# Kernel optimization log

Measured on AMD Instinct MI355X. Metric: run time of the kernel, lower is better.

The kernel has to match this reference:

```python
import jax, jax.numpy as jnp
import numpy as np

HID, H, D = 128, 4, 32
NB, NP, NC = 60000, 2000, 4000
EM, EP, EI = 150000, 300000, 150000


def segment_softmax(logits, seg, n):
    # logits: [E, H], seg: [E] destination ids
    m = jax.ops.segment_max(logits, seg, num_segments=n)
    m = jnp.where(jnp.isfinite(m), m, 0.0)  # guard empty segments
    e = jnp.exp(logits - m[seg])
    s = jax.ops.segment_sum(e, seg, num_segments=n)
    return e / (s[seg] + 1e-16)


def layer_norm(x, g, b):
    mu = x.mean(-1, keepdims=True)
    v = ((x - mu) ** 2).mean(-1, keepdims=True)
    return (x - mu) / jnp.sqrt(v + 1e-5) * g + b


def setup_inputs():
    key = jax.random.key(0)
    ks = jax.random.split(key, 40)
    i = iter(range(40))
    nrm = lambda shape, s=1.0: jax.random.normal(ks[next(i)], shape, jnp.float32) * s
    w = lambda shape: nrm(shape, 0.05)
    inp = {
        'x_ball': nrm((NB, HID)),
        'x_player': nrm((NP, HID)),
        'x_context': nrm((NC, HID)),
        'em': jnp.stack([jax.random.randint(ks[next(i)], (EM,), 0, NP),
                         jax.random.randint(ks[next(i)], (EM,), 0, NB)]),
        'ep': jnp.stack([jax.random.randint(ks[next(i)], (EP,), 0, NB),
                         jax.random.randint(ks[next(i)], (EP,), 0, NB)]),
        'ei': jnp.stack([jax.random.randint(ks[next(i)], (EI,), 0, NB),
                         jax.random.randint(ks[next(i)], (EI,), 0, NC)]),
        'ea_p': nrm((EP, 1)),
        # GATv2Conv (player -matchup-> ball)
        'g_Wl': w((HID, HID)), 'g_Wr': w((HID, HID)), 'g_att': w((H, D)), 'g_b': jnp.zeros((HID,), jnp.float32),
        # TransformerConv (ball -recent_precedes-> ball), edge_dim=1
        't_Wq': w((HID, HID)), 't_bq': jnp.zeros((HID,), jnp.float32),
        't_Wk': w((HID, HID)), 't_bk': jnp.zeros((HID,), jnp.float32),
        't_Wv': w((HID, HID)), 't_bv': jnp.zeros((HID,), jnp.float32),
        't_We': w((1, HID)),
        't_Wskip': w((HID, HID)), 't_bskip': jnp.zeros((HID,), jnp.float32),
        # SAGEConv mean (ball -informs-> context)
        's_Wl': w((HID, HID)), 's_bl': jnp.zeros((HID,), jnp.float32), 's_Wr': w((HID, HID)),
        # per-type LayerNorms (only applied to types produced by the conv)
        'ln_ball_g': jnp.ones((HID,), jnp.float32), 'ln_ball_b': jnp.zeros((HID,), jnp.float32),
        'ln_ctx_g': jnp.ones((HID,), jnp.float32), 'ln_ctx_b': jnp.zeros((HID,), jnp.float32),
    }
    return inp


def reference(x_ball, x_player, x_context, em, ep, ei, ea_p,
              g_Wl, g_Wr, g_att, g_b,
              t_Wq, t_bq, t_Wk, t_bk, t_Wv, t_bv, t_We, t_Wskip, t_bskip,
              s_Wl, s_bl, s_Wr,
              ln_ball_g, ln_ball_b, ln_ctx_g, ln_ctx_b):
    # ---- GATv2Conv: player -> ball ----
    src, dst = em[0], em[1]
    xl = (x_player @ g_Wl).reshape(NP, H, D)   # src transform
    xr = (x_ball @ g_Wr).reshape(NB, H, D)     # dst transform
    e = xl[src] + xr[dst]                      # [EM, H, D]
    e = jnp.where(e > 0, e, 0.2 * e)           # leaky_relu(0.2)
    logit = jnp.einsum('ehd,hd->eh', e, g_att)
    alpha = segment_softmax(logit, dst, NB)
    gat = jax.ops.segment_sum(xl[src] * alpha[..., None], dst, num_segments=NB)
    gat = gat.reshape(NB, HID) + g_b

    # ---- TransformerConv: ball -> ball, edge_dim=1 ----
    src, dst = ep[0], ep[1]
    q = (x_ball @ t_Wq + t_bq).reshape(NB, H, D)
    k = (x_ball @ t_Wk + t_bk).reshape(NB, H, D)
    v = (x_ball @ t_Wv + t_bv).reshape(NB, H, D)
    ee = (ea_p @ t_We).reshape(EP, H, D)       # lin_edge (no bias)
    kj = k[src] + ee
    logit = jnp.einsum('ehd,ehd->eh', q[dst], kj) / jnp.sqrt(jnp.float32(D))
    alpha = segment_softmax(logit, dst, NB)
    tr = jax.ops.segment_sum((v[src] + ee) * alpha[..., None], dst, num_segments=NB)
    tr = tr.reshape(NB, HID) + x_ball @ t_Wskip + t_bskip  # root/skip connection

    # ---- SAGEConv mean: ball -> context ----
    src, dst = ei[0], ei[1]
    summ = jax.ops.segment_sum(x_ball[src], dst, num_segments=NC)
    cnt = jax.ops.segment_sum(jnp.ones((EI,), jnp.float32), dst, num_segments=NC)
    mean = summ / jnp.maximum(cnt, 1.0)[:, None]
    sage = mean @ s_Wl + s_bl + x_context @ s_Wr

    # ---- HeteroConv aggr='sum' + residual + per-type LayerNorm ----
    ball_out = layer_norm(gat + tr + x_ball, ln_ball_g, ln_ball_b)
    ctx_out = layer_norm(sage + x_context, ln_ctx_g, ln_ctx_b)
    # 'player' receives no messages -> passed through unchanged
    return (ball_out, ctx_out, x_player)
```

## Files before the change

### kernel.cpp

```cpp
#include <hip/hip_runtime.h>
#include <hip/hip_bf16.h>

#define NB 60000
#define NP 2000
#define NC 4000
#define EM_N 150000
#define EP_N 300000
#define EI_N 150000
#define POOL_N (EM_N + EP_N + EI_N)
#define SEG_TOT (NB + NB + NC)
#define SCAN_BLK 1024
#define NPART ((SEG_TOT + SCAN_BLK - 1) / SCAN_BLK)
#define BALL_TILES ((NB + 63) / 64)
#define PLYR_TILES ((NP + 63) / 64)
#define CTX_TILES ((NC + 63) / 64)
#define TPB 4
#define BW_CH ((BALL_TILES + TPB - 1) / TPB)
#define PW_CH ((PLYR_TILES + TPB - 1) / TPB)
#define CW_CH ((CTX_TILES + TPB - 1) / TPB)
#define GEMM_BLKS (6 * BW_CH + PW_CH + CW_CH)
#define FILL_BLKS ((POOL_N + 255) / 256)
#define CONVB ((NB * 16 + 255) / 256)
#define CONVC ((NC * 16 + 255) / 256)
#define CONVP ((NP * 16 + 255) / 256)
#define HIST_BLKS (FILL_BLKS + CONVB + CONVC + CONVP)
#define BBALL ((NB + 3) / 4)

#define QSCALE (0.17677669529663687f * 1.4426950408889634f)
#define LOG2E 1.4426950408889634f

typedef __hip_bfloat16 bf16;
typedef unsigned int u32;
typedef __attribute__((ext_vector_type(8))) short s8v;
typedef __attribute__((ext_vector_type(4))) float f4v;

__device__ __forceinline__ short f2bs(float f) {
    bf16 h = __float2bfloat16(f);
    return __builtin_bit_cast(short, h);
}
__device__ __forceinline__ float bsToF(short s) {
    return __builtin_bit_cast(float, ((unsigned)(unsigned short)s) << 16);
}
__device__ __forceinline__ float loF(u32 v) { return bsToF((short)(v & 0xffff)); }
__device__ __forceinline__ float hiF(u32 v) { return bsToF((short)(v >> 16)); }
__device__ __forceinline__ u32 packbf(float a, float b) {
    return (u32)(unsigned short)f2bs(a) | ((u32)(unsigned short)f2bs(b) << 16);
}
__device__ __forceinline__ void gl_lds16(const void* g, void* l) {
    __builtin_amdgcn_global_load_lds((const __attribute__((address_space(1))) void*)g,
                                     (__attribute__((address_space(3))) void*)l, 16, 0, 0);
}

__global__ void hist_wt_copy_kernel(const int* __restrict__ em, const int* __restrict__ ep,
                                    const int* __restrict__ ei, int* __restrict__ counts,
                                    int* __restrict__ ranks,
                                    const float* __restrict__ W0, const float* __restrict__ W1,
                                    const float* __restrict__ W2, const float* __restrict__ W3,
                                    const float* __restrict__ W4, const float* __restrict__ W5,
                                    const float* __restrict__ W6, const float* __restrict__ W7,
                                    ushort* __restrict__ Wt,
                                    const float* __restrict__ x_ball, const float* __restrict__ x_context,
                                    const float* __restrict__ x_player,
                                    u32* __restrict__ xbB, u32* __restrict__ xbC, u32* __restrict__ xbP,
                                    float* __restrict__ out) {
    if (blockIdx.x >= FILL_BLKS) {
        int b2 = blockIdx.x - FILL_BLKS;
        if (b2 < CONVB) {
            int idx = b2 * 256 + threadIdx.x;
            const float4* p = (const float4*)(x_ball + (size_t)idx * 8);
            float4 u = p[0], v = p[1];
            ((uint4*)xbB)[idx] = make_uint4(packbf(u.x, u.y), packbf(u.z, u.w),
                                            packbf(v.x, v.y), packbf(v.z, v.w));
        } else if (b2 < CONVB + CONVC) {
            int idx = (b2 - CONVB) * 256 + threadIdx.x;
            const float4* p = (const float4*)(x_context + (size_t)idx * 8);
            float4 u = p[0], v = p[1];
            ((uint4*)xbC)[idx] = make_uint4(packbf(u.x, u.y), packbf(u.z, u.w),
                                            packbf(v.x, v.y), packbf(v.z, v.w));
        } else {
            int idx = (b2 - CONVB - CONVC) * 256 + threadIdx.x;
            const float4* p = (const float4*)(x_player + (size_t)idx * 8);
            float4 u = p[0], v = p[1];
            ((uint4*)xbP)[idx] = make_uint4(packbf(u.x, u.y), packbf(u.z, u.w),
                                            packbf(v.x, v.y), packbf(v.z, v.w));
            float4* po = (float4*)(out + (size_t)(NB + NC) * 128 + (size_t)idx * 8);
            po[0] = u; po[1] = v;
        }
        return;
    }
    int t = blockIdx.x * 256 + threadIdx.x;
    if (t < 8 * 16384) {
        int w = t >> 14, r = t & 16383, k = r >> 7, n = r & 127;
        const float* W = (w == 0) ? W0 : (w == 1) ? W1 : (w == 2) ? W2 : (w == 3) ? W3
                       : (w == 4) ? W4 : (w == 5) ? W5 : (w == 6) ? W6 : W7;
        int sc = (n >> 5) * 32 + ((n & 1) << 4) + ((n & 31) >> 1);
        Wt[w * 16384 + (k >> 3) * 1024 + sc * 8 + (k & 7)] = (unsigned short)f2bs(W[k * 128 + n]);
    }
    if (t < EM_N) ranks[t] = atomicAdd(&counts[em[EM_N + t]], 1);
    else if (t < EM_N + EP_N) ranks[t] = atomicAdd(&counts[NB + ep[EP_N + (t - EM_N)]], 1);
    else if (t < POOL_N) ranks[t] = atomicAdd(&counts[2 * NB + ei[EI_N + (t - EM_N - EP_N)]], 1);
}

__global__ void scan_fused_kernel(const int* __restrict__ counts, int* __restrict__ offsets,
                                  int* __restrict__ gbase) {
    __shared__ int sd[256];
    __shared__ int sbase;
    int b = blockIdx.x, tid = threadIdx.x;
    int base = b * SCAN_BLK + tid * 4;
    int v[4]; int ts = 0;
#pragma unroll
    for (int j = 0; j < 4; j++) { int idx = base + j; v[j] = (idx < SEG_TOT) ? counts[idx] : 0; ts += v[j]; }
    sd[tid] = ts;
    for (int off = 1; off < 256; off <<= 1) {
        __syncthreads(); int t = (tid >= off) ? sd[tid - off] : 0;
        __syncthreads(); sd[tid] += t;
    }
    __syncthreads();
    if (tid == 255) sbase = atomicAdd(gbase, sd[255]);
    __syncthreads();
    int run = sd[tid] - ts + sbase;
#pragma unroll
    for (int j = 0; j < 4; j++) {
        int idx = base + j;
        if (idx < SEG_TOT) offsets[idx] = run;
        run += v[j];
    }
}

__global__ __launch_bounds__(256) void gemm6_fill_kernel(
    const u32* __restrict__ xbB, const u32* __restrict__ xbP, const u32* __restrict__ xbC,
    const float* __restrict__ Aball, const float* __restrict__ Actx,
    const ushort* __restrict__ Wt,
    const float* __restrict__ bq, const float* __restrict__ bk,
    const float* __restrict__ bv_, const float* __restrict__ bskip, const float* __restrict__ bl,
    u32* __restrict__ xrP, u32* __restrict__ qP, u32* __restrict__ kvP,
    u32* __restrict__ skipP, u32* __restrict__ xlP, u32* __restrict__ xwP,
    u32* __restrict__ ctxlinP,
    const int* __restrict__ em, const int* __restrict__ ep, const int* __restrict__ ei,
    const float* __restrict__ ea_p, const int* __restrict__ offsets,
    const int* __restrict__ ranks, int2* __restrict__ pool) {
    __shared__ ushort lds[16384];
    if (blockIdx.x >= GEMM_BLKS) {
        int t = (blockIdx.x - GEMM_BLKS) * 256 + threadIdx.x;
        int seg, s; float ea = 0.f;
        if (t < EM_N) { s = em[t]; seg = em[EM_N + t]; }
        else if (t < EM_N + EP_N) { int e = t - EM_N; s = ep[e]; seg = NB + ep[EP_N + e]; ea = ea_p[e]; }
        else if (t < POOL_N) { int e = t - EM_N - EP_N; s = ei[e]; seg = 2 * NB + ei[EI_N + e]; }
        else return;
        int pos = offsets[seg] + ranks[t];
        pool[pos] = make_int2(s, __float_as_int(ea));
        return;
    }
    const int tid = threadIdx.x;
    const int lane = tid & 63;
    const int wv = tid >> 6;
    const int quad = lane >> 4, l16 = lane & 15;

    int bid = blockIdx.x;
    int w, tile0, ntiles, M;
    const u32* A;
    if (bid < 6 * BW_CH) {
        int widx = bid / BW_CH;
        w = (widx < 5) ? widx : 6;
        int chunk = bid - widx * BW_CH;
        tile0 = chunk * TPB; ntiles = min(TPB, BALL_TILES - tile0); M = NB; A = xbB;
    } else if (bid < 6 * BW_CH + PW_CH) {
        w = 5; int chunk = bid - 6 * BW_CH;
        tile0 = chunk * TPB; ntiles = min(TPB, PLYR_TILES - tile0); M = NP; A = xbP;
    } else {
        w = 7; int chunk = bid - 6 * BW_CH - PW_CH;
        tile0 = chunk * TPB; ntiles = min(TPB, CTX_TILES - tile0); M = NC; A = xbC;
    }
    u32* op; const float* bp = nullptr; const float* resid = nullptr; float scale = 1.f;
    int ostride = 64, omul = 1, ooff = 0;
    switch (w) {
        case 0: op = xrP; break;
        case 1: op = qP; bp = bq; scale = QSCALE; break;
        case 2: op = kvP; bp = bk; ostride = 128; omul = 2; ooff = 0; break;
        case 3: op = kvP; bp = bv_; ostride = 128; omul = 2; ooff = 1; break;
        case 4: op = skipP; bp = bskip; resid = Aball; break;
        case 5: op = xlP; break;
        case 6: op = xwP; break;
        default: op = ctxlinP; bp = bl; resid = Actx; break;
    }

    {
        const ushort* src = Wt + w * 16384;
#pragma unroll
        for (int p = 0; p < 8; p++)
            gl_lds16(src + (size_t)(p * 256 + tid) * 8, lds + p * 2048 + wv * 512);
    }

    float2 bias2[4];
#pragma unroll
    for (int t = 0; t < 4; t++)
        bias2[t] = bp ? ((const float2*)bp)[t * 16 + l16] : make_float2(0.f, 0.f);

    s8v aCur[4], aNext[4];
    {
        int r0 = tile0 * 64 + wv * 16 + l16; if (r0 >= M) r0 = M - 1;
        const s8v* ap = (const s8v*)(A + (size_t)r0 * 64 + quad * 4);
#pragma unroll
        for (int kt = 0; kt < 4; kt++) aCur[kt] = ap[kt * 4];
    }
    __syncthreads();

    for (int ti = 0; ti < ntiles; ti++) {
        int tilebase = (tile0 + ti) * 64;
        if (ti + 1 < ntiles) {
            int rn = tilebase + 64 + wv * 16 + l16; if (rn >= M) rn = M - 1;
            const s8v* ap = (const s8v*)(A + (size_t)rn * 64 + quad * 4);
#pragma unroll
            for (int kt = 0; kt < 4; kt++) aNext[kt] = ap[kt * 4];
        }
        const int mbase = tilebase + wv * 16;
#pragma unroll
        for (int t = 0; t < 4; t++) {
            f4v alo = {0.f, 0.f, 0.f, 0.f}, ahi = {0.f, 0.f, 0.f, 0.f};
#pragma unroll
            for (int kt = 0; kt < 4; kt++) {
                s8v blo = *(const s8v*)(lds + (kt * 4 + quad) * 1024 + (t * 32 + l16) * 8);
                s8v bhi = *(const s8v*)(lds + (kt * 4 + quad) * 1024 + (t * 32 + 16 + l16) * 8);
                alo = __builtin_amdgcn_mfma_f32_16x16x32_bf16(aCur[kt], blo, alo, 0, 0, 0);
                ahi = __builtin_amdgcn_mfma_f32_16x16x32_bf16(aCur[kt], bhi, ahi, 0, 0, 0);
            }
#pragma unroll
            for (int r = 0; r < 4; r++) {
                int row = mbase + quad * 4 + r;
                if (row < M) {
                    float vlo = (alo[r] + bias2[t].x) * scale;
                    float vhi = (ahi[r] + bias2[t].y) * scale;
                    if (resid) {
                        float2 x2 = ((const float2*)resid)[(size_t)row * 64 + t * 16 + l16];
                        vlo += x2.x; vhi += x2.y;
                    }
                    op[(size_t)row * ostride + (size_t)(t * 16 + l16) * omul + ooff] = packbf(vlo, vhi);
                }
            }
        }
#pragma unroll
        for (int i = 0; i < 4; i++) aCur[i] = aNext[i];
    }
}

__device__ __forceinline__ void gat_batch(const u32 xv[4], const bool ok[4],
                                          float xr0, float xr1, float attx, float atty,
                                          float& n0, float& n1, float& deg) {
    float p[4], xa[4], xb[4];
#pragma unroll
    for (int i = 0; i < 4; i++) {
        xa[i] = loF(xv[i]); xb[i] = hiF(xv[i]);
        float u0 = xa[i] + xr0; u0 = u0 > 0.f ? u0 : 0.2f * u0;
        float u1 = xb[i] + xr1; u1 = u1 > 0.f ? u1 : 0.2f * u1;
        p[i] = u0 * attx + u1 * atty;
    }
#pragma unroll
    for (int m = 1; m <= 8; m <<= 1) {
#pragma unroll
        for (int i = 0; i < 4; i++) p[i] += __shfl_xor(p[i], m);
    }
#pragma unroll
    for (int i = 0; i < 4; i++) {
        p[i] = ok[i] ? exp2f(p[i]) : 0.f;
        n0 += p[i] * xa[i]; n1 += p[i] * xb[i]; deg += p[i];
    }
}

__device__ __forceinline__ void tr_batch(const uint2 kv[4], const float ea[4], const bool ok[4],
                                         float q0, float q1, float dw,
                                         float& sv0, float& sv1, float& spe, float& det) {
    float p[4];
#pragma unroll
    for (int i = 0; i < 4; i++) p[i] = q0 * loF(kv[i].x) + q1 * hiF(kv[i].x);
#pragma unroll
    for (int m = 1; m <= 8; m <<= 1) {
#pragma unroll
        for (int i = 0; i < 4; i++) p[i] += __shfl_xor(p[i], m);
    }
#pragma unroll
    for (int i = 0; i < 4; i++) {
        p[i] = ok[i] ? exp2f(p[i] + ea[i] * dw) : 0.f;
        sv0 += p[i] * loF(kv[i].y); sv1 += p[i] * hiF(kv[i].y);
        spe += p[i] * ea[i]; det += p[i];
    }
}

__global__ __launch_bounds__(256) void ball_sage_kernel(
    const u32* __restrict__ xlP, const u32* __restrict__ xrP, const u32* __restrict__ qP,
    const uint2* __restrict__ kvP, const u32* __restrict__ skipP, const u32* __restrict__ xwP,
    const u32* __restrict__ ctxlinP,
    const float* __restrict__ g_att, const float* __restrict__ g_b, const float* __restrict__ We,
    const int* __restrict__ offsets, const int* __restrict__ counts,
    const int2* __restrict__ pool,
    const float* __restrict__ ln_g, const float* __restrict__ ln_b,
    const float* __restrict__ cg, const float* __restrict__ cb,
    float* __restrict__ out) {
    __shared__ float part[4][128];
    const int wv = threadIdx.x >> 6, l = threadIdx.x & 63;

    if (blockIdx.x >= BBALL) {
        int c = blockIdx.x - BBALL;
        int beg = offsets[2 * NB + c], cnt = counts[2 * NB + c];
        float s0 = 0.f, s1 = 0.f;
        int j = wv;
        if (j < cnt) {
            int i0 = pool[beg + j].x;
            int idx1 = (j + 4 < cnt) ? beg + j + 4 : 0;
            int i1 = pool[idx1].x;
            u32 x0 = xwP[(size_t)i0 * 64 + l];
            u32 x1 = xwP[(size_t)i1 * 64 + l];
            for (; j < cnt; j += 4) {
                int idx2 = (j + 8 < cnt) ? beg + j + 8 : 0;
                int i2 = pool[idx2].x;
                s0 += loF(x0); s1 += hiF(x0);
                x0 = x1;
                x1 = xwP[(size_t)i2 * 64 + l];
            }
        }
        part[wv][l * 2] = s0; part[wv][l * 2 + 1] = s1;
        __syncthreads();
        if (wv == 0) {
            float m = fmaxf((float)cnt, 1.f);
            u32 cl = ctxlinP[(size_t)c * 64 + l];
            float v0 = (part[0][l * 2] + part[1][l * 2] + part[2][l * 2] + part[3][l * 2]) / m + loF(cl);
            float v1 = (part[0][l * 2 + 1] + part[1][l * 2 + 1] + part[2][l * 2 + 1] + part[3][l * 2 + 1]) / m + hiF(cl);
            float s = v0 + v1;
#pragma unroll
            for (int m2 = 1; m2 <= 32; m2 <<= 1) s += __shfl_xor(s, m2);
            float mu = s * (1.f / 128.f);
            float d0 = v0 - mu, d1 = v1 - mu;
            float qv = d0 * d0 + d1 * d1;
#pragma unroll
            for (int m2 = 1; m2 <= 32; m2 <<= 1) qv += __shfl_xor(qv, m2);
            float inv = rsqrtf(qv * (1.f / 128.f) + 1e-5f);
            float2 g2 = ((const float2*)cg)[l];
            float2 b2 = ((const float2*)cb)[l];
            ((float2*)out)[(size_t)(NB + c) * 64 + l] =
                make_float2(d0 * inv * g2.x + b2.x, d1 * inv * g2.y + b2.y);
        }
        return;
    }

    const int d = blockIdx.x * 4 + wv;
    const size_t rowD = (size_t)d * 64;
    const int ds = __builtin_amdgcn_readfirstlane(d);

    u32 xr2 = xrP[rowD + l];
    u32 q2 = qP[rowD + l];
    u32 sk = skipP[rowD + l];

    const int begG = offsets[ds], cntG = counts[ds];
    const int begT = offsets[NB + ds], cntT = counts[NB + ds];
    int gS[8];
#pragma unroll
    for (int i = 0; i < 8; i++) { int idx = (i < cntG) ? begG + i : 0; gS[i] = pool[idx].x; }
    int tS[8]; float tE[8];
#pragma unroll
    for (int i = 0; i < 8; i++) {
        int idx = (i < cntT) ? begT + i : 0;
        int2 pr = pool[idx]; tS[i] = pr.x; tE[i] = __int_as_float(pr.y);
    }

    u32 gx[8];
    if (cntG > 0) {
#pragma unroll
        for (int i = 0; i < 4; i++) gx[i] = xlP[(size_t)gS[i] * 64 + l];
        if (cntG > 4) {
#pragma unroll
            for (int i = 4; i < 8; i++) gx[i] = xlP[(size_t)gS[i] * 64 + l];
        }
    }
    uint2 kva[8];
    if (cntT > 0) {
#pragma unroll
        for (int i = 0; i < 4; i++) kva[i] = kvP[(size_t)tS[i] * 64 + l];
        if (cntT > 4) {
#pragma unroll
            for (int i = 4; i < 8; i++) kva[i] = kvP[(size_t)tS[i] * 64 + l];
        }
    }

    float q0 = loF(q2), q1 = hiF(q2);
    float2 we = ((const float2*)We)[l];
    float dw = q0 * we.x + q1 * we.y;
#pragma unroll
    for (int m = 1; m <= 8; m <<= 1) dw += __shfl_xor(dw, m);

    float2 attv = ((const float2*)g_att)[l];
    float attx = attv.x * LOG2E, atty = attv.y * LOG2E;
    float xr0 = loF(xr2), xr1 = hiF(xr2);
    float n0 = 0.f, n1 = 0.f, deg = 0.f;
    if (cntG > 0) {
        bool ok[4];
#pragma unroll
        for (int i = 0; i < 4; i++) ok[i] = (i < cntG);
        gat_batch(&gx[0], ok, xr0, xr1, attx, atty, n0, n1, deg);
        if (cntG > 4) {
            bool ok2[4];
#pragma unroll
            for (int i = 0; i < 4; i++) ok2[i] = (4 + i < cntG);
            gat_batch(&gx[4], ok2, xr0, xr1, attx, atty, n0, n1, deg);
        }
        for (int j = 8; j < cntG; j += 4) {
            bool ok3[4]; u32 xv[4];
#pragma unroll
            for (int i = 0; i < 4; i++) {
                ok3[i] = (j + i < cntG);
                int idx = ok3[i] ? begG + j + i : 0;
                xv[i] = xlP[(size_t)pool[idx].x * 64 + l];
            }
            gat_batch(xv, ok3, xr0, xr1, attx, atty, n0, n1, deg);
        }
    }
    float gat0 = n0 / (deg + 1e-16f), gat1 = n1 / (deg + 1e-16f);

    float sv0 = 0.f, sv1 = 0.f, spe = 0.f, det = 0.f;
    if (cntT > 0) {
        bool ok[4];
#pragma unroll
        for (int i = 0; i < 4; i++) ok[i] = (i < cntT);
        tr_batch(&kva[0], &tE[0], ok, q0, q1, dw, sv0, sv1, spe, det);
        if (cntT > 4) {
            bool ok2[4];
#pragma unroll
            for (int i = 0; i < 4; i++) ok2[i] = (4 + i < cntT);
            tr_batch(&kva[4], &tE[4], ok2, q0, q1, dw, sv0, sv1, spe, det);
        }
        for (int j = 8; j < cntT; j += 4) {
            bool ok3[4]; uint2 kv[4]; float ea[4];
#pragma unroll
            for (int i = 0; i < 4; i++) {
                ok3[i] = (j + i < cntT);
                int idx = ok3[i] ? begT + j + i : 0;
                int2 pr = pool[idx];
                ea[i] = __int_as_float(pr.y);
                kv[i] = kvP[(size_t)pr.x * 64 + l];
            }
            tr_batch(kv, ea, ok3, q0, q1, dw, sv0, sv1, spe, det);
        }
    }
    float tr0 = (sv0 + spe * we.x) / (det + 1e-16f);
    float tr1 = (sv1 + spe * we.y) / (det + 1e-16f);

    float2 gb2 = ((const float2*)g_b)[l];
    float val0 = loF(sk) + gb2.x + gat0 + tr0;
    float val1 = hiF(sk) + gb2.y + gat1 + tr1;
    float s = val0 + val1;
#pragma unroll
    for (int m = 1; m <= 32; m <<= 1) s += __shfl_xor(s, m);
    float mu = s * (1.f / 128.f);
    float d0 = val0 - mu, d1 = val1 - mu;
    float qv = d0 * d0 + d1 * d1;
#pragma unroll
    for (int m = 1; m <= 32; m <<= 1) qv += __shfl_xor(qv, m);
    float inv = rsqrtf(qv * (1.f / 128.f) + 1e-5f);
    float2 g2 = ((const float2*)ln_g)[l];
    float2 b2 = ((const float2*)ln_b)[l];
    ((float2*)out)[rowD + l] = make_float2(d0 * inv * g2.x + b2.x, d1 * inv * g2.y + b2.y);
}

extern "C" void kernel_launch(void* const* d_in, const int* in_sizes, int n_in,
                              void* d_out, int out_size, void* d_ws, size_t ws_size,
                              hipStream_t stream) {
    const float* x_ball = (const float*)d_in[0];
    const float* x_player = (const float*)d_in[1];
    const float* x_context = (const float*)d_in[2];
    const int* em = (const int*)d_in[3];
    const int* ep = (const int*)d_in[4];
    const int* ei = (const int*)d_in[5];
    const float* ea_p = (const float*)d_in[6];
    const float* g_Wl = (const float*)d_in[7];
    const float* g_Wr = (const float*)d_in[8];
    const float* g_att = (const float*)d_in[9];
    const float* g_b = (const float*)d_in[10];
    const float* t_Wq = (const float*)d_in[11];
    const float* t_bq = (const float*)d_in[12];
    const float* t_Wk = (const float*)d_in[13];
    const float* t_bk = (const float*)d_in[14];
    const float* t_Wv = (const float*)d_in[15];
    const float* t_bv = (const float*)d_in[16];
    const float* t_We = (const float*)d_in[17];
    const float* t_Wskip = (const float*)d_in[18];
    const float* t_bskip = (const float*)d_in[19];
    const float* s_Wl = (const float*)d_in[20];
    const float* s_bl = (const float*)d_in[21];
    const float* s_Wr = (const float*)d_in[22];
    const float* ln_ball_g = (const float*)d_in[23];
    const float* ln_ball_b = (const float*)d_in[24];
    const float* ln_ctx_g = (const float*)d_in[25];
    const float* ln_ctx_b = (const float*)d_in[26];
    float* out = (float*)d_out;

    float* ws = (float*)d_ws;
    size_t o = 0;
    int* counts = (int*)(ws + o);   o += SEG_TOT;
    int* gbase = (int*)(ws + o);    o += 1;
    int* offsets = (int*)(ws + o);  o += SEG_TOT;
    int* ranks = (int*)(ws + o);    o += POOL_N;
    if (o & 1) o++;
    int2* pool = (int2*)(ws + o);   o += (size_t)POOL_N * 2;
    o = (o + 3) & ~(size_t)3;
    ushort* Wt = (ushort*)(ws + o); o += (8 * 16384) / 2;
    u32* xbB = (u32*)(ws + o);      o += (size_t)NB * 64;
    u32* xbC = (u32*)(ws + o);      o += (size_t)NC * 64;
    u32* xbP = (u32*)(ws + o);      o += (size_t)NP * 64;
    u32* xlP = (u32*)(ws + o);      o += (size_t)NP * 64;
    u32* xrP = (u32*)(ws + o);      o += (size_t)NB * 64;
    u32* qP = (u32*)(ws + o);       o += (size_t)NB * 64;
    u32* skipP = (u32*)(ws + o);    o += (size_t)NB * 64;
    u32* xwP = (u32*)(ws + o);      o += (size_t)NB * 64;
    u32* ctxlinP = (u32*)(ws + o);  o += (size_t)NC * 64;
    if (o & 1) o++;
    u32* kvP = (u32*)(ws + o);      o += (size_t)NB * 128;

    dim3 blk(256);
    hipMemsetAsync(counts, 0, (SEG_TOT + 1) * sizeof(int), stream);
    hist_wt_copy_kernel<<<HIST_BLKS, blk, 0, stream>>>(
        em, ep, ei, counts, ranks, g_Wr, t_Wq, t_Wk, t_Wv, t_Wskip, g_Wl, s_Wl, s_Wr, Wt,
        x_ball, x_context, x_player, xbB, xbC, xbP, out);
    scan_fused_kernel<<<NPART, blk, 0, stream>>>(counts, offsets, gbase);
    gemm6_fill_kernel<<<GEMM_BLKS + FILL_BLKS, blk, 0, stream>>>(
        xbB, xbP, xbC, x_ball, x_context, Wt, t_bq, t_bk, t_bv, t_bskip, s_bl,
        xrP, qP, kvP, skipP, xlP, xwP, ctxlinP, em, ep, ei, ea_p, offsets, ranks, pool);
    ball_sage_kernel<<<BBALL + NC, blk, 0, stream>>>(
        xlP, xrP, qP, (const uint2*)kvP, skipP, xwP, ctxlinP, g_att, g_b, t_We,
        offsets, counts, pool, ln_ball_g, ln_ball_b, ln_ctx_g, ln_ctx_b, out);
}
```

Before: 303.7 us.

## Split GEMM to one tile per block, de-interleave K/V layout, regroup prep kernels

The GEMM kernel now handles one 64-row tile per block instead of four tiles with register prefetch of the next A tile. This raises block count but reloads the weight slab into LDS once per tile. The K/V buffer changes from interleaved per-element pairs to separate K and V halves per row, so the attention gather issues two u32 loads instead of one uint2. The histogram now runs alone, and the weight transpose and bf16 conversion move into the scan kernel. This shortens the atomic-heavy histogram launch and lets the conversion work overlap with the scan.

```diff
diff --git a/kernel.cpp b/kernel.cpp
--- a/kernel.cpp
+++ b/kernel.cpp
@@ -14,16 +14,12 @@
 #define BALL_TILES ((NB + 63) / 64)
 #define PLYR_TILES ((NP + 63) / 64)
 #define CTX_TILES ((NC + 63) / 64)
-#define TPB 4
-#define BW_CH ((BALL_TILES + TPB - 1) / TPB)
-#define PW_CH ((PLYR_TILES + TPB - 1) / TPB)
-#define CW_CH ((CTX_TILES + TPB - 1) / TPB)
-#define GEMM_BLKS (6 * BW_CH + PW_CH + CW_CH)
+#define GEMM_BLKS (6 * BALL_TILES + PLYR_TILES + CTX_TILES)
 #define FILL_BLKS ((POOL_N + 255) / 256)
 #define CONVB ((NB * 16 + 255) / 256)
 #define CONVC ((NC * 16 + 255) / 256)
 #define CONVP ((NP * 16 + 255) / 256)
-#define HIST_BLKS (FILL_BLKS + CONVB + CONVC + CONVP)
+#define PREP_BLKS (NPART + 512 + CONVB + CONVC + CONVP)
 #define BBALL ((NB + 3) / 4)
 
 #define QSCALE (0.17677669529663687f * 1.4426950408889634f)
@@ -51,79 +47,82 @@
                                      (__attribute__((address_space(3))) void*)l, 16, 0, 0);
 }
 
-__global__ void hist_wt_copy_kernel(const int* __restrict__ em, const int* __restrict__ ep,
-                                    const int* __restrict__ ei, int* __restrict__ counts,
-                                    int* __restrict__ ranks,
-                                    const float* __restrict__ W0, const float* __restrict__ W1,
-                                    const float* __restrict__ W2, const float* __restrict__ W3,
-                                    const float* __restrict__ W4, const float* __restrict__ W5,
-                                    const float* __restrict__ W6, const float* __restrict__ W7,
-                                    ushort* __restrict__ Wt,
-                                    const float* __restrict__ x_ball, const float* __restrict__ x_context,
-                                    const float* __restrict__ x_player,
-                                    u32* __restrict__ xbB, u32* __restrict__ xbC, u32* __restrict__ xbP,
-                                    float* __restrict__ out) {
-    if (blockIdx.x >= FILL_BLKS) {
-        int b2 = blockIdx.x - FILL_BLKS;
-        if (b2 < CONVB) {
-            int idx = b2 * 256 + threadIdx.x;
-            const float4* p = (const float4*)(x_ball + (size_t)idx * 8);
-            float4 u = p[0], v = p[1];
-            ((uint4*)xbB)[idx] = make_uint4(packbf(u.x, u.y), packbf(u.z, u.w),
-                                            packbf(v.x, v.y), packbf(v.z, v.w));
-        } else if (b2 < CONVB + CONVC) {
-            int idx = (b2 - CONVB) * 256 + threadIdx.x;
-            const float4* p = (const float4*)(x_context + (size_t)idx * 8);
-            float4 u = p[0], v = p[1];
-            ((uint4*)xbC)[idx] = make_uint4(packbf(u.x, u.y), packbf(u.z, u.w),
-                                            packbf(v.x, v.y), packbf(v.z, v.w));
-        } else {
-            int idx = (b2 - CONVB - CONVC) * 256 + threadIdx.x;
-            const float4* p = (const float4*)(x_player + (size_t)idx * 8);
-            float4 u = p[0], v = p[1];
-            ((uint4*)xbP)[idx] = make_uint4(packbf(u.x, u.y), packbf(u.z, u.w),
-                                            packbf(v.x, v.y), packbf(v.z, v.w));
-            float4* po = (float4*)(out + (size_t)(NB + NC) * 128 + (size_t)idx * 8);
-            po[0] = u; po[1] = v;
+__global__ void hist_kernel(const int* __restrict__ em, const int* __restrict__ ep,
+                            const int* __restrict__ ei, int* __restrict__ counts,
+                            int* __restrict__ ranks) {
+    int t = blockIdx.x * 256 + threadIdx.x;
+    if (t < EM_N) ranks[t] = atomicAdd(&counts[em[EM_N + t]], 1);
+    else if (t < EM_N + EP_N) ranks[t] = atomicAdd(&counts[NB + ep[EP_N + (t - EM_N)]], 1);
+    else if (t < POOL_N) ranks[t] = atomicAdd(&counts[2 * NB + ei[EI_N + (t - EM_N - EP_N)]], 1);
+}
+
+__global__ void prepscan_kernel(const int* __restrict__ counts, int* __restrict__ offsets,
+                                int* __restrict__ gbase,
+                                const float* __restrict__ W0, const float* __restrict__ W1,
+                                const float* __restrict__ W2, const float* __restrict__ W3,
+                                const float* __restrict__ W4, const float* __restrict__ W5,
+                                const float* __restrict__ W6, const float* __restrict__ W7,
+                                ushort* __restrict__ Wt,
+                                const float* __restrict__ x_ball, const float* __restrict__ x_context,
+                                const float* __restrict__ x_player,
+                                u32* __restrict__ xbB, u32* __restrict__ xbC, u32* __restrict__ xbP,
+                                float* __restrict__ out) {
+    __shared__ int sd[256];
+    __shared__ int sbase;
+    if (blockIdx.x < NPART) {
+        int b = blockIdx.x, tid = threadIdx.x;
+        int base = b * SCAN_BLK + tid * 4;
+        int v[4]; int ts = 0;
+#pragma unroll
+        for (int j = 0; j < 4; j++) { int idx = base + j; v[j] = (idx < SEG_TOT) ? counts[idx] : 0; ts += v[j]; }
+        sd[tid] = ts;
+        for (int off = 1; off < 256; off <<= 1) {
+            __syncthreads(); int t = (tid >= off) ? sd[tid - off] : 0;
+            __syncthreads(); sd[tid] += t;
+        }
+        __syncthreads();
+        if (tid == 255) sbase = atomicAdd(gbase, sd[255]);
+        __syncthreads();
+        int run = sd[tid] - ts + sbase;
+#pragma unroll
+        for (int j = 0; j < 4; j++) {
+            int idx = base + j;
+            if (idx < SEG_TOT) offsets[idx] = run;
+            run += v[j];
         }
         return;
     }
-    int t = blockIdx.x * 256 + threadIdx.x;
-    if (t < 8 * 16384) {
+    int b2 = blockIdx.x - NPART;
+    if (b2 < 512) {
+        int t = b2 * 256 + threadIdx.x;
         int w = t >> 14, r = t & 16383, k = r >> 7, n = r & 127;
         const float* W = (w == 0) ? W0 : (w == 1) ? W1 : (w == 2) ? W2 : (w == 3) ? W3
                        : (w == 4) ? W4 : (w == 5) ? W5 : (w == 6) ? W6 : W7;
         int sc = (n >> 5) * 32 + ((n & 1) << 4) + ((n & 31) >> 1);
         Wt[w * 16384 + (k >> 3) * 1024 + sc * 8 + (k & 7)] = (unsigned short)f2bs(W[k * 128 + n]);
-    }
-    if (t < EM_N) ranks[t] = atomicAdd(&counts[em[EM_N + t]], 1);
-    else if (t < EM_N + EP_N) ranks[t] = atomicAdd(&counts[NB + ep[EP_N + (t - EM_N)]], 1);
-    else if (t < POOL_N) ranks[t] = atomicAdd(&counts[2 * NB + ei[EI_N + (t - EM_N - EP_N)]], 1);
-}
-
-__global__ void scan_fused_kernel(const int* __restrict__ counts, int* __restrict__ offsets,
-                                  int* __restrict__ gbase) {
-    __shared__ int sd[256];
-    __shared__ int sbase;
-    int b = blockIdx.x, tid = threadIdx.x;
-    int base = b * SCAN_BLK + tid * 4;
-    int v[4]; int ts = 0;
-#pragma unroll
-    for (int j = 0; j < 4; j++) { int idx = base + j; v[j] = (idx < SEG_TOT) ? counts[idx] : 0; ts += v[j]; }
-    sd[tid] = ts;
-    for (int off = 1; off < 256; off <<= 1) {
-        __syncthreads(); int t = (tid >= off) ? sd[tid - off] : 0;
-        __syncthreads(); sd[tid] += t;
-    }
-    __syncthreads();
-    if (tid == 255) sbase = atomicAdd(gbase, sd[255]);
-    __syncthreads();
-    int run = sd[tid] - ts + sbase;
-#pragma unroll
-    for (int j = 0; j < 4; j++) {
-        int idx = base + j;
-        if (idx < SEG_TOT) offsets[idx] = run;
-        run += v[j];
+        return;
+    }
+    int b3 = b2 - 512;
+    if (b3 < CONVB) {
+        int idx = b3 * 256 + threadIdx.x;
+        const float4* p = (const float4*)(x_ball + (size_t)idx * 8);
+        float4 u = p[0], v = p[1];
+        ((uint4*)xbB)[idx] = make_uint4(packbf(u.x, u.y), packbf(u.z, u.w),
+                                        packbf(v.x, v.y), packbf(v.z, v.w));
+    } else if (b3 < CONVB + CONVC) {
+        int idx = (b3 - CONVB) * 256 + threadIdx.x;
+        const float4* p = (const float4*)(x_context + (size_t)idx * 8);
+        float4 u = p[0], v = p[1];
+        ((uint4*)xbC)[idx] = make_uint4(packbf(u.x, u.y), packbf(u.z, u.w),
+                                        packbf(v.x, v.y), packbf(v.z, v.w));
+    } else {
+        int idx = (b3 - CONVB - CONVC) * 256 + threadIdx.x;
+        const float4* p = (const float4*)(x_player + (size_t)idx * 8);
+        float4 u = p[0], v = p[1];
+        ((uint4*)xbP)[idx] = make_uint4(packbf(u.x, u.y), packbf(u.z, u.w),
+                                        packbf(v.x, v.y), packbf(v.z, v.w));
+        float4* po = (float4*)(out + (size_t)(NB + NC) * 128 + (size_t)idx * 8);
+        po[0] = u; po[1] = v;
     }
 }
 
@@ -157,27 +156,24 @@
     const int quad = lane >> 4, l16 = lane & 15;
 
     int bid = blockIdx.x;
-    int w, tile0, ntiles, M;
+    int w, tile, M;
     const u32* A;
-    if (bid < 6 * BW_CH) {
-        int widx = bid / BW_CH;
+    if (bid < 6 * BALL_TILES) {
+        int widx = bid / BALL_TILES;
         w = (widx < 5) ? widx : 6;
-        int chunk = bid - widx * BW_CH;
-        tile0 = chunk * TPB; ntiles = min(TPB, BALL_TILES - tile0); M = NB; A = xbB;
-    } else if (bid < 6 * BW_CH + PW_CH) {
-        w = 5; int chunk = bid - 6 * BW_CH;
-        tile0 = chunk * TPB; ntiles = min(TPB, PLYR_TILES - tile0); M = NP; A = xbP;
+        tile = bid - widx * BALL_TILES; M = NB; A = xbB;
+    } else if (bid < 6 * BALL_TILES + PLYR_TILES) {
+        w = 5; tile = bid - 6 * BALL_TILES; M = NP; A = xbP;
     } else {
-        w = 7; int chunk = bid - 6 * BW_CH - PW_CH;
-        tile0 = chunk * TPB; ntiles = min(TPB, CTX_TILES - tile0); M = NC; A = xbC;
+        w = 7; tile = bid - 6 * BALL_TILES - PLYR_TILES; M = NC; A = xbC;
     }
     u32* op; const float* bp = nullptr; const float* resid = nullptr; float scale = 1.f;
-    int ostride = 64, omul = 1, ooff = 0;
+    int ostride = 64, ooff = 0;
     switch (w) {
         case 0: op = xrP; break;
         case 1: op = qP; bp = bq; scale = QSCALE; break;
-        case 2: op = kvP; bp = bk; ostride = 128; omul = 2; ooff = 0; break;
-        case 3: op = kvP; bp = bv_; ostride = 128; omul = 2; ooff = 1; break;
+        case 2: op = kvP; bp = bk; ostride = 128; ooff = 0; break;
+        case 3: op = kvP; bp = bv_; ostride = 128; ooff = 64; break;
         case 4: op = skipP; bp = bskip; resid = Aball; break;
         case 5: op = xlP; break;
         case 6: op = xwP; break;
@@ -191,55 +187,43 @@
             gl_lds16(src + (size_t)(p * 256 + tid) * 8, lds + p * 2048 + wv * 512);
     }
 
+    s8v a[4];
+    {
+        int r0 = tile * 64 + wv * 16 + l16; if (r0 >= M) r0 = M - 1;
+        const s8v* ap = (const s8v*)(A + (size_t)r0 * 64 + quad * 4);
+#pragma unroll
+        for (int kt = 0; kt < 4; kt++) a[kt] = ap[kt * 4];
+    }
     float2 bias2[4];
 #pragma unroll
     for (int t = 0; t < 4; t++)
         bias2[t] = bp ? ((const float2*)bp)[t * 16 + l16] : make_float2(0.f, 0.f);
-
-    s8v aCur[4], aNext[4];
-    {
-        int r0 = tile0 * 64 + wv * 16 + l16; if (r0 >= M) r0 = M - 1;
-        const s8v* ap = (const s8v*)(A + (size_t)r0 * 64 + quad * 4);
-#pragma unroll
-        for (int kt = 0; kt < 4; kt++) aCur[kt] = ap[kt * 4];
-    }
     __syncthreads();
 
-    for (int ti = 0; ti < ntiles; ti++) {
-        int tilebase = (tile0 + ti) * 64;
-        if (ti + 1 < ntiles) {
-            int rn = tilebase + 64 + wv * 16 + l16; if (rn >= M) rn = M - 1;
-            const s8v* ap = (const s8v*)(A + (size_t)rn * 64 + quad * 4);
-#pragma unroll
-            for (int kt = 0; kt < 4; kt++) aNext[kt] = ap[kt * 4];
-        }
-        const int mbase = tilebase + wv * 16;
-#pragma unroll
-        for (int t = 0; t < 4; t++) {
-            f4v alo = {0.f, 0.f, 0.f, 0.f}, ahi = {0.f, 0.f, 0.f, 0.f};
-#pragma unroll
-            for (int kt = 0; kt < 4; kt++) {
-                s8v blo = *(const s8v*)(lds + (kt * 4 + quad) * 1024 + (t * 32 + l16) * 8);
-                s8v bhi = *(const s8v*)(lds + (kt * 4 + quad) * 1024 + (t * 32 + 16 + l16) * 8);
-                alo = __builtin_amdgcn_mfma_f32_16x16x32_bf16(aCur[kt], blo, alo, 0, 0, 0);
-                ahi = __builtin_amdgcn_mfma_f32_16x16x32_bf16(aCur[kt], bhi, ahi, 0, 0, 0);
+    const int mbase = tile * 64 + wv * 16;
+#pragma unroll
+    for (int t = 0; t < 4; t++) {
+        f4v alo = {0.f, 0.f, 0.f, 0.f}, ahi = {0.f, 0.f, 0.f, 0.f};
+#pragma unroll
+        for (int kt = 0; kt < 4; kt++) {
+            s8v blo = *(const s8v*)(lds + (kt * 4 + quad) * 1024 + (t * 32 + l16) * 8);
+            s8v bhi = *(const s8v*)(lds + (kt * 4 + quad) * 1024 + (t * 32 + 16 + l16) * 8);
+            alo = __builtin_amdgcn_mfma_f32_16x16x32_bf16(a[kt], blo, alo, 0, 0, 0);
+            ahi = __builtin_amdgcn_mfma_f32_16x16x32_bf16(a[kt], bhi, ahi, 0, 0, 0);
+        }
+#pragma unroll
+        for (int r = 0; r < 4; r++) {
+            int row = mbase + quad * 4 + r;
+            if (row < M) {
+                float vlo = (alo[r] + bias2[t].x) * scale;
+                float vhi = (ahi[r] + bias2[t].y) * scale;
+                if (resid) {
+                    float2 x2 = ((const float2*)resid)[(size_t)row * 64 + t * 16 + l16];
+                    vlo += x2.x; vhi += x2.y;
+                }
+                op[(size_t)row * ostride + ooff + t * 16 + l16] = packbf(vlo, vhi);
             }
-#pragma unroll
-            for (int r = 0; r < 4; r++) {
-                int row = mbase + quad * 4 + r;
-                if (row < M) {
-                    float vlo = (alo[r] + bias2[t].x) * scale;
-                    float vhi = (ahi[r] + bias2[t].y) * scale;
-                    if (resid) {
-                        float2 x2 = ((const float2*)resid)[(size_t)row * 64 + t * 16 + l16];
-                        vlo += x2.x; vhi += x2.y;
-                    }
-                    op[(size_t)row * ostride + (size_t)(t * 16 + l16) * omul + ooff] = packbf(vlo, vhi);
-                }
-            }
-        }
-#pragma unroll
-        for (int i = 0; i < 4; i++) aCur[i] = aNext[i];
+        }
     }
 }
 
@@ -266,12 +250,13 @@
     }
 }
 
-__device__ __forceinline__ void tr_batch(const uint2 kv[4], const float ea[4], const bool ok[4],
+__device__ __forceinline__ void tr_batch(const u32 kk[4], const u32 vv[4],
+                                         const float ea[4], const bool ok[4],
                                          float q0, float q1, float dw,
                                          float& sv0, float& sv1, float& spe, float& det) {
     float p[4];
 #pragma unroll
-    for (int i = 0; i < 4; i++) p[i] = q0 * loF(kv[i].x) + q1 * hiF(kv[i].x);
+    for (int i = 0; i < 4; i++) p[i] = q0 * loF(kk[i]) + q1 * hiF(kk[i]);
 #pragma unroll
     for (int m = 1; m <= 8; m <<= 1) {
 #pragma unroll
@@ -280,14 +265,14 @@
 #pragma unroll
     for (int i = 0; i < 4; i++) {
         p[i] = ok[i] ? exp2f(p[i] + ea[i] * dw) : 0.f;
-        sv0 += p[i] * loF(kv[i].y); sv1 += p[i] * hiF(kv[i].y);
+        sv0 += p[i] * loF(vv[i]); sv1 += p[i] * hiF(vv[i]);
         spe += p[i] * ea[i]; det += p[i];
     }
 }
 
 __global__ __launch_bounds__(256) void ball_sage_kernel(
     const u32* __restrict__ xlP, const u32* __restrict__ xrP, const u32* __restrict__ qP,
-    const uint2* __restrict__ kvP, const u32* __restrict__ skipP, const u32* __restrict__ xwP,
+    const u32* __restrict__ kvP, const u32* __restrict__ skipP, const u32* __restrict__ xwP,
     const u32* __restrict__ ctxlinP,
     const float* __restrict__ g_att, const float* __restrict__ g_b, const float* __restrict__ We,
     const int* __restrict__ offsets, const int* __restrict__ counts,
@@ -370,13 +355,19 @@
             for (int i = 4; i < 8; i++) gx[i] = xlP[(size_t)gS[i] * 64 + l];
         }
     }
-    uint2 kva[8];
+    u32 kk[8], vv[8];
     if (cntT > 0) {
 #pragma unroll
-        for (int i = 0; i < 4; i++) kva[i] = kvP[(size_t)tS[i] * 64 + l];
+        for (int i = 0; i < 4; i++) {
+            kk[i] = kvP[(size_t)tS[i] * 128 + l];
+            vv[i] = kvP[(size_t)tS[i] * 128 + 64 + l];
+        }
         if (cntT > 4) {
 #pragma unroll
-            for (int i = 4; i < 8; i++) kva[i] = kvP[(size_t)tS[i] * 64 + l];
+            for (int i = 4; i < 8; i++) {
+                kk[i] = kvP[(size_t)tS[i] * 128 + l];
+                vv[i] = kvP[(size_t)tS[i] * 128 + 64 + l];
+            }
         }
     }
 
@@ -419,24 +410,25 @@
         bool ok[4];
 #pragma unroll
         for (int i = 0; i < 4; i++) ok[i] = (i < cntT);
-        tr_batch(&kva[0], &tE[0], ok, q0, q1, dw, sv0, sv1, spe, det);
+        tr_batch(&kk[0], &vv[0], &tE[0], ok, q0, q1, dw, sv0, sv1, spe, det);
         if (cntT > 4) {
             bool ok2[4];
 #pragma unroll
             for (int i = 0; i < 4; i++) ok2[i] = (4 + i < cntT);
-            tr_batch(&kva[4], &tE[4], ok2, q0, q1, dw, sv0, sv1, spe, det);
+            tr_batch(&kk[4], &vv[4], &tE[4], ok2, q0, q1, dw, sv0, sv1, spe, det);
         }
         for (int j = 8; j < cntT; j += 4) {
-            bool ok3[4]; uint2 kv[4]; float ea[4];
+            bool ok3[4]; u32 kt2[4], vt2[4]; float ea[4];
 #pragma unroll
             for (int i = 0; i < 4; i++) {
                 ok3[i] = (j + i < cntT);
                 int idx = ok3[i] ? begT + j + i : 0;
                 int2 pr = pool[idx];
                 ea[i] = __int_as_float(pr.y);
-                kv[i] = kvP[(size_t)pr.x * 64 + l];
+                kt2[i] = kvP[(size_t)pr.x * 128 + l];
+                vt2[i] = kvP[(size_t)pr.x * 128 + 64 + l];
             }
-            tr_batch(kv, ea, ok3, q0, q1, dw, sv0, sv1, spe, det);
+            tr_batch(kt2, vt2, ea, ok3, q0, q1, dw, sv0, sv1, spe, det);
         }
     }
     float tr0 = (sv0 + spe * we.x) / (det + 1e-16f);
@@ -515,14 +507,14 @@
 
     dim3 blk(256);
     hipMemsetAsync(counts, 0, (SEG_TOT + 1) * sizeof(int), stream);
-    hist_wt_copy_kernel<<<HIST_BLKS, blk, 0, stream>>>(
-        em, ep, ei, counts, ranks, g_Wr, t_Wq, t_Wk, t_Wv, t_Wskip, g_Wl, s_Wl, s_Wr, Wt,
+    hist_kernel<<<FILL_BLKS, blk, 0, stream>>>(em, ep, ei, counts, ranks);
+    prepscan_kernel<<<PREP_BLKS, blk, 0, stream>>>(
+        counts, offsets, gbase, g_Wr, t_Wq, t_Wk, t_Wv, t_Wskip, g_Wl, s_Wl, s_Wr, Wt,
         x_ball, x_context, x_player, xbB, xbC, xbP, out);
-    scan_fused_kernel<<<NPART, blk, 0, stream>>>(counts, offsets, gbase);
     gemm6_fill_kernel<<<GEMM_BLKS + FILL_BLKS, blk, 0, stream>>>(
         xbB, xbP, xbC, x_ball, x_context, Wt, t_bq, t_bk, t_bv, t_bskip, s_bl,
         xrP, qP, kvP, skipP, xlP, xwP, ctxlinP, em, ep, ei, ea_p, offsets, ranks, pool);
     ball_sage_kernel<<<BBALL + NC, blk, 0, stream>>>(
-        xlP, xrP, qP, (const uint2*)kvP, skipP, xwP, ctxlinP, g_att, g_b, t_We,
+        xlP, xrP, qP, kvP, skipP, xwP, ctxlinP, g_att, g_b, t_We,
         offsets, counts, pool, ln_ball_g, ln_ball_b, ln_ctx_g, ln_ctx_b, out);
 }
```

Measured after the change: 289.3 us. -4.8%, faster.
